# Kernel tuning notes

Measured on AMD Instinct MI355X. Metric: run time of the kernel, lower is better.

## Reference

```python
import jax, jax.numpy as jnp
import numpy as np

WS = 4          # window size per axis
HEADS = 3
HEAD_DIM = 32
DIM = 96
DISP = WS // 2  # displacement for shifted windows


def _make_mask(axis):
    # (w^3, w^3) additive mask, -inf across the wrap-around boundary on `axis`
    m = np.zeros((WS, WS, WS, WS, WS, WS), dtype=np.float32)
    d = DISP
    if axis == 0:
        m[-d:, :, :, :-d, :, :] = -np.inf
        m[:-d, :, :, -d:, :, :] = -np.inf
    elif axis == 1:
        m[:, -d:, :, :, :-d, :] = -np.inf
        m[:, :-d, :, :, -d:, :] = -np.inf
    else:
        m[:, :, -d:, :, :, :-d] = -np.inf
        m[:, :, :-d, :, :, -d:] = -np.inf
    return jnp.asarray(m.reshape(WS**3, WS**3))


def setup_inputs() -> dict:
    key = jax.random.key(0)
    k1, k2, k3, k4 = jax.random.split(key, 4)
    inner = HEADS * HEAD_DIM
    x = jax.random.normal(k1, (1, 64, 64, 64, DIM), dtype=jnp.float32)
    w_qkv = jax.random.normal(k2, (3 * inner, DIM), dtype=jnp.float32) * 0.02
    w_out = jax.random.normal(k3, (DIM, inner), dtype=jnp.float32) * 0.02
    b_out = jax.random.normal(k4, (DIM,), dtype=jnp.float32) * 0.02
    return {
        'x': x, 'w_qkv': w_qkv, 'w_out': w_out, 'b_out': b_out,
        'x_mask': _make_mask(0), 'y_mask': _make_mask(1), 'z_mask': _make_mask(2),
    }


def _forward(x, w_qkv, w_out, b_out, x_mask, y_mask, z_mask):
    scale = HEAD_DIM ** -0.5
    b, nx, ny, nz, _ = x.shape
    nwx, nwy, nwz = nx // WS, ny // WS, nz // WS
    seq = WS ** 3
    # cyclic shift by -displacement
    x = jnp.roll(x, shift=(-DISP, -DISP, -DISP), axis=(1, 2, 3))
    qkv = jnp.einsum('bxyzc,oc->bxyzo', x, w_qkv)
    q, k, v = jnp.split(qkv, 3, axis=-1)

    def win(t):  # -> (b, h, n_windows, seq, d)
        t = t.reshape(b, nwx, WS, nwy, WS, nwz, WS, HEADS, HEAD_DIM)
        t = t.transpose(0, 7, 1, 3, 5, 2, 4, 6, 8)
        return t.reshape(b, HEADS, nwx * nwy * nwz, seq, HEAD_DIM)

    q, k, v = win(q), win(k), win(v)
    dots = jnp.einsum('bhwid,bhwjd->bhwij', q, k) * scale

    # shifted-window masking (faithful to original einops relabeling, incl.
    # the final mislabeled rearrange which permutes the window grid)
    d = dots.reshape(b, HEADS, nwx, nwy, nwz, seq, seq)
    d = d.transpose(0, 1, 3, 4, 2, 5, 6)          # (b,h,ny,nz,nx,i,j)
    d = d.at[:, :, :, :, -1].add(x_mask)
    d = d.transpose(0, 1, 4, 3, 2, 5, 6)          # (b,h,nx,nz,ny,i,j)
    d = d.at[:, :, :, :, -1].add(y_mask)
    d = d.transpose(0, 1, 2, 4, 3, 5, 6)          # (b,h,nx,ny,nz,i,j)
    d = d.transpose(0, 1, 4, 2, 3, 5, 6)          # original's final rearrange bug
    dots = d.reshape(b, HEADS, nwx * nwy * nwz, seq, seq)

    attn = jax.nn.softmax(dots, axis=-1)
    out = jnp.einsum('bhwij,bhwjd->bhwid', attn, v)
    # un-window
    out = out.reshape(b, HEADS, nwx, nwy, nwz, WS, WS, WS, HEAD_DIM)
    out = out.transpose(0, 2, 5, 3, 6, 4, 7, 1, 8).reshape(b, nx, ny, nz, HEADS * HEAD_DIM)
    out = jnp.einsum('bxyzc,oc->bxyzo', out, w_out) + b_out
    # cyclic back shift
    return jnp.roll(out, shift=(DISP, DISP, DISP), axis=(1, 2, 3))


def reference(x, w_qkv, w_out, b_out, x_mask, y_mask, z_mask):
    return _forward(x, w_qkv, w_out, b_out, x_mask, y_mask, z_mask)
```

## Files before the change

### kernel.cpp

```cpp
#include <hip/hip_runtime.h>
#include <hip/hip_bf16.h>


using bf4   = __attribute__((ext_vector_type(4))) short;
using bf8   = __attribute__((ext_vector_type(8))) short;
using f32x4 = __attribute__((ext_vector_type(4))) float;

#define SW      100
#define WQ_ROWS 288
#define W_ROWS  384
#define W_SHORTS (W_ROWS * SW)

__device__ __forceinline__ short f2b(float f) {
  __hip_bfloat16 h = __float2bfloat16(f);
  return *reinterpret_cast<short*>(&h);
}
__device__ __forceinline__ bf4 pk4(const f32x4& a) {
  bf4 s; s[0] = f2b(a[0]); s[1] = f2b(a[1]); s[2] = f2b(a[2]); s[3] = f2b(a[3]);
  return s;
}
__device__ __forceinline__ bf4 pk4s(const f32x4& a, float sc) {
  bf4 s; s[0] = f2b(a[0] * sc); s[1] = f2b(a[1] * sc);
  s[2] = f2b(a[2] * sc); s[3] = f2b(a[3] * sc);
  return s;
}
__device__ __forceinline__ bf8 cvt8(const float4& a, const float4& b) {
  bf8 o;
  o[0] = f2b(a.x); o[1] = f2b(a.y); o[2] = f2b(a.z); o[3] = f2b(a.w);
  o[4] = f2b(b.x); o[5] = f2b(b.y); o[6] = f2b(b.z); o[7] = f2b(b.w);
  return o;
}

#if __has_builtin(__builtin_amdgcn_mfma_f32_16x16x16bf16_1k)
__device__ __forceinline__ f32x4 mfma16(bf4 a, bf4 b, f32x4 c) {
  return __builtin_amdgcn_mfma_f32_16x16x16bf16_1k(a, b, c, 0, 0, 0);
}
#elif __has_builtin(__builtin_amdgcn_mfma_f32_16x16x16_bf16)
__device__ __forceinline__ f32x4 mfma16(bf4 a, bf4 b, f32x4 c) {
  return __builtin_amdgcn_mfma_f32_16x16x16_bf16(a, b, c, 0, 0, 0);
}
#else
__device__ __forceinline__ f32x4 mfma16(bf4 a, bf4 b, f32x4 c) {
  asm("v_mfma_f32_16x16x16_bf16 %0, %1, %2, %0" : "+v"(c) : "v"(a), "v"(b));
  return c;
}
#endif

#if __has_builtin(__builtin_amdgcn_exp2f)
__device__ __forceinline__ float exp2n(float x) { return __builtin_amdgcn_exp2f(x); }
#else
__device__ __forceinline__ float exp2n(float x) {
  float r; asm("v_exp_f32 %0, %1" : "=v"(r) : "v"(x)); return r;
}
#endif

__global__ void prep_weights(const float* __restrict__ wq, const float* __restrict__ wo,
                             short* __restrict__ wpk) {
  int i = blockIdx.x * 256 + threadIdx.x;
  if (i >= W_SHORTS) return;
  int row = i / SW, c = i - row * SW;
  const float QS = 0.17677669529663687f * 1.4426950408889634f;
  float v = 0.f;
  if (c < 96) {
    if (row < 96)           v = wq[row * 96 + c] * QS;
    else if (row < WQ_ROWS) v = wq[row * 96 + c];
    else                    v = wo[(row - WQ_ROWS) * 96 + c];
  }
  wpk[i] = f2b(v);
}

__global__ __launch_bounds__(256)
__attribute__((amdgpu_waves_per_eu(1, 2)))
void fused_swin3d(const float* __restrict__ x,
                  const short* __restrict__ wpk,
                  const float* __restrict__ bo,
                  float* __restrict__ out) {
  __shared__ __align__(16) short ls_w[W_SHORTS];

  const int tid = threadIdx.x;
  const float4* wsrc = reinterpret_cast<const float4*>(wpk);
  #pragma unroll
  for (int i = 0; i < 19; ++i) {
    int c = i * 256 + tid;
    if (c < W_SHORTS / 8)
      *reinterpret_cast<float4*>(&ls_w[c * 8]) = wsrc[c];
  }

  const int wbase = ((int)blockIdx.x * 4 + (tid >> 6)) * 2;
  const int lane = tid & 63;
  const int lr   = lane & 15;
  const int kg   = lane >> 4;
  const int sy = (lr >> 2) & 3, sz = lr & 3;
  const int ch0 = kg * 8;
  const short* ls_wo = ls_w + WQ_ROWS * SW;

  __syncthreads();

  #pragma unroll
  for (int wi = 0; wi < 2; ++wi) {
    const int w = wbase + wi;
    const int p = w >> 8, q = (w >> 4) & 15, r = w & 15;

    bf4 qn[4][6], kn[4][6], vn[4][6];

    #pragma unroll
    for (int sc = 0; sc < 4; ++sc) {
      const int gx1 = (q * 4 + sc + 2) & 63, gy1 = (r * 4 + sy + 2) & 63, gz1 = (p * 4 + sz + 2) & 63;
      const size_t b1 = (size_t)((gx1 * 64 + gy1) * 64 + gz1) * 96;

      float4 xa0 = *reinterpret_cast<const float4*>(&x[b1 +  0 + ch0]);
      float4 xa1 = *reinterpret_cast<const float4*>(&x[b1 + 32 + ch0]);
      float4 xa2 = *reinterpret_cast<const float4*>(&x[b1 + 64 + ch0]);
      float4 xa3 = *reinterpret_cast<const float4*>(&x[b1 +  0 + ch0 + 4]);
      float4 xa4 = *reinterpret_cast<const float4*>(&x[b1 + 32 + ch0 + 4]);
      float4 xa5 = *reinterpret_cast<const float4*>(&x[b1 + 64 + ch0 + 4]);

      bf8 x1[3];
      x1[0] = cvt8(xa0, xa3); x1[1] = cvt8(xa1, xa4); x1[2] = cvt8(xa2, xa5);

      #pragma unroll
      for (int n = 0; n < 12; ++n) {
        f32x4 acc = {0.f, 0.f, 0.f, 0.f};
        const short* wrow = &ls_w[(n * 16 + lr) * SW + ch0];
        acc = __builtin_amdgcn_mfma_f32_16x16x32_bf16(*reinterpret_cast<const bf8*>(wrow +  0), x1[0], acc, 0, 0, 0);
        acc = __builtin_amdgcn_mfma_f32_16x16x32_bf16(*reinterpret_cast<const bf8*>(wrow + 32), x1[1], acc, 0, 0, 0);
        acc = __builtin_amdgcn_mfma_f32_16x16x32_bf16(*reinterpret_cast<const bf8*>(wrow + 64), x1[2], acc, 0, 0, 0);
        if (n < 6) qn[sc][n] = pk4(acc);
        else       kn[sc][n - 6] = pk4(acc);
      }
    }

    #pragma unroll
    for (int sc = 0; sc < 4; ++sc) {
      const int gx2 = (p * 4 + sc + 2) & 63, gy2 = (q * 4 + sy + 2) & 63, gz2 = (r * 4 + sz + 2) & 63;
      const size_t b2 = (size_t)((gx2 * 64 + gy2) * 64 + gz2) * 96;

      float4 xb0 = *reinterpret_cast<const float4*>(&x[b2 +  0 + ch0]);
      float4 xb1 = *reinterpret_cast<const float4*>(&x[b2 + 32 + ch0]);
      float4 xb2 = *reinterpret_cast<const float4*>(&x[b2 + 64 + ch0]);
      float4 xb3 = *reinterpret_cast<const float4*>(&x[b2 +  0 + ch0 + 4]);
      float4 xb4 = *reinterpret_cast<const float4*>(&x[b2 + 32 + ch0 + 4]);
      float4 xb5 = *reinterpret_cast<const float4*>(&x[b2 + 64 + ch0 + 4]);

      bf8 x2[3];
      x2[0] = cvt8(xb0, xb3); x2[1] = cvt8(xb1, xb4); x2[2] = cvt8(xb2, xb5);

      #pragma unroll
      for (int n = 0; n < 6; ++n) {
        f32x4 acc = {0.f, 0.f, 0.f, 0.f};
        const short* wrow = &ls_w[(192 + n * 16 + lr) * SW + ch0];
        acc = __builtin_amdgcn_mfma_f32_16x16x32_bf16(x2[0], *reinterpret_cast<const bf8*>(wrow +  0), acc, 0, 0, 0);
        acc = __builtin_amdgcn_mfma_f32_16x16x32_bf16(x2[1], *reinterpret_cast<const bf8*>(wrow + 32), acc, 0, 0, 0);
        acc = __builtin_amdgcn_mfma_f32_16x16x32_bf16(x2[2], *reinterpret_cast<const bf8*>(wrow + 64), acc, 0, 0, 0);
        vn[sc][n] = pk4(acc);
      }
    }

    const bool mx = (q == 15), my = (r == 15);
    const bool killy = my && ((lr >= 8) != (kg >= 2));

    #pragma unroll
    for (int qc = 0; qc < 4; ++qc) {
      f32x4 osw[6];
      #pragma unroll
      for (int c = 0; c < 6; ++c) osw[c] = (f32x4){0.f, 0.f, 0.f, 0.f};

      #pragma unroll
      for (int h = 0; h < 3; ++h) {
        f32x4 sv[4];
        __builtin_amdgcn_s_setprio(1);
        #pragma unroll
        for (int nj = 0; nj < 4; ++nj) {
          f32x4 z = {0.f, 0.f, 0.f, 0.f};
          z = mfma16(kn[nj][2 * h + 0], qn[qc][2 * h + 0], z);
          sv[nj] = mfma16(kn[nj][2 * h + 1], qn[qc][2 * h + 1], z);
        }
        __builtin_amdgcn_s_setprio(0);
        float ps[4];
        #pragma unroll
        for (int nj = 0; nj < 4; ++nj) {
          const bool kill = killy || (mx && ((qc >= 2) != (nj >= 2)));
          #pragma unroll
          for (int t = 0; t < 4; ++t)
            sv[nj][t] = kill ? 0.f : exp2n(sv[nj][t]);
          ps[nj] = (sv[nj][0] + sv[nj][1]) + (sv[nj][2] + sv[nj][3]);
        }
        float sum = (ps[0] + ps[1]) + (ps[2] + ps[3]);
        sum += __shfl_xor(sum, 16);
        sum += __shfl_xor(sum, 32);
        const float inv = 1.f / sum;
        bf4 pb[4];
        #pragma unroll
        for (int t = 0; t < 4; ++t) pb[t] = pk4s(sv[t], inv);
        __builtin_amdgcn_s_setprio(1);
        #pragma unroll
        for (int nc = 0; nc < 2; ++nc)
          #pragma unroll
          for (int t = 0; t < 4; ++t)
            osw[2 * h + nc] = mfma16(vn[t][2 * h + nc], pb[t], osw[2 * h + nc]);
        __builtin_amdgcn_s_setprio(0);
      }

      bf4 ofr[6];
      #pragma unroll
      for (int c = 0; c < 6; ++c) ofr[c] = pk4(osw[c]);

      const int gx2 = (p * 4 + qc + 2) & 63, gy2 = (q * 4 + sy + 2) & 63, gz2 = (r * 4 + sz + 2) & 63;
      const size_t b2 = (size_t)((gx2 * 64 + gy2) * 64 + gz2) * 96;
      #pragma unroll
      for (int no = 0; no < 6; ++no) {
        f32x4 acc = {0.f, 0.f, 0.f, 0.f};
        const short* wr = &ls_wo[(no * 16 + lr) * SW + kg * 4];
        #pragma unroll
        for (int c = 0; c < 6; ++c) {
          bf4 wa = *reinterpret_cast<const bf4*>(wr + c * 16);
          acc = mfma16(wa, ofr[c], acc);
        }
        const float4 bb = *reinterpret_cast<const float4*>(&bo[no * 16 + kg * 4]);
        float4 o4;
        o4.x = acc[0] + bb.x; o4.y = acc[1] + bb.y;
        o4.z = acc[2] + bb.z; o4.w = acc[3] + bb.w;
        *reinterpret_cast<float4*>(&out[b2 + no * 16 + kg * 4]) = o4;
      }
    }
  }
}

extern "C" void kernel_launch(void* const* d_in, const int* in_sizes, int n_in,
                              void* d_out, int out_size, void* d_ws, size_t ws_size,
                              hipStream_t stream) {
  const float* x  = (const float*)d_in[0];
  const float* wq = (const float*)d_in[1];
  const float* wo = (const float*)d_in[2];
  const float* bo = (const float*)d_in[3];

  short* wpk = (short*)d_ws;

  prep_weights<<<(W_SHORTS + 255) / 256, 256, 0, stream>>>(wq, wo, wpk);
  fused_swin3d<<<512, 256, 0, stream>>>(x, wpk, bo, (float*)d_out);
}
```

Measured before the change: 88.67 us.

## Use cheap bf16 packing and merge QK^T into single 16x16x32 MFMAs

Replaces per-element __float2bfloat16 conversions with a bit-add rounding trick that packs two floats per 32-bit word, cutting ALU work in every conversion. It also packs Q and K fragments as bf8 pairs, so each head's score computation uses one 16x16x32 MFMA instead of two chained 16x16x16 MFMAs. The rounding drops NaN handling and ties-to-even behaviour, which slightly changes numerics. The packing relies on the head-dim halves lining up with the K layout of the 32-wide MFMA.

Result: slower. 92.78 us (+4.6%).

```diff
diff --git a/kernel.cpp b/kernel.cpp
--- a/kernel.cpp
+++ b/kernel.cpp
@@ -11,25 +11,44 @@
 #define W_ROWS  384
 #define W_SHORTS (W_ROWS * SW)
 
+__device__ __forceinline__ unsigned rnd16(float f) {
+  return __builtin_bit_cast(unsigned, f) + 0x8000u;
+}
+__device__ __forceinline__ unsigned pk2u(float a, float b) {
+  return (rnd16(a) >> 16) | (rnd16(b) & 0xffff0000u);
+}
+__device__ __forceinline__ bf4 pk4f(const f32x4& v) {
+  union { unsigned u[2]; bf4 s; } t;
+  t.u[0] = pk2u(v[0], v[1]);
+  t.u[1] = pk2u(v[2], v[3]);
+  return t.s;
+}
+__device__ __forceinline__ bf4 pk4fs(const f32x4& v, float sc) {
+  f32x4 w = { v[0] * sc, v[1] * sc, v[2] * sc, v[3] * sc };
+  return pk4f(w);
+}
+__device__ __forceinline__ bf8 pk8f(const f32x4& a, const f32x4& b) {
+  union { unsigned u[4]; bf8 s; } t;
+  t.u[0] = pk2u(a[0], a[1]);
+  t.u[1] = pk2u(a[2], a[3]);
+  t.u[2] = pk2u(b[0], b[1]);
+  t.u[3] = pk2u(b[2], b[3]);
+  return t.s;
+}
+__device__ __forceinline__ bf8 cvt8f(const float4& a, const float4& b) {
+  union { unsigned u[4]; bf8 s; } t;
+  t.u[0] = pk2u(a.x, a.y);
+  t.u[1] = pk2u(a.z, a.w);
+  t.u[2] = pk2u(b.x, b.y);
+  t.u[3] = pk2u(b.z, b.w);
+  return t.s;
+}
 __device__ __forceinline__ short f2b(float f) {
   __hip_bfloat16 h = __float2bfloat16(f);
   return *reinterpret_cast<short*>(&h);
 }
-__device__ __forceinline__ bf4 pk4(const f32x4& a) {
-  bf4 s; s[0] = f2b(a[0]); s[1] = f2b(a[1]); s[2] = f2b(a[2]); s[3] = f2b(a[3]);
-  return s;
-}
-__device__ __forceinline__ bf4 pk4s(const f32x4& a, float sc) {
-  bf4 s; s[0] = f2b(a[0] * sc); s[1] = f2b(a[1] * sc);
-  s[2] = f2b(a[2] * sc); s[3] = f2b(a[3] * sc);
-  return s;
-}
-__device__ __forceinline__ bf8 cvt8(const float4& a, const float4& b) {
-  bf8 o;
-  o[0] = f2b(a.x); o[1] = f2b(a.y); o[2] = f2b(a.z); o[3] = f2b(a.w);
-  o[4] = f2b(b.x); o[5] = f2b(b.y); o[6] = f2b(b.z); o[7] = f2b(b.w);
-  return o;
-}
+
+#define mfma32 __builtin_amdgcn_mfma_f32_16x16x32_bf16
 
 #if __has_builtin(__builtin_amdgcn_mfma_f32_16x16x16bf16_1k)
 __device__ __forceinline__ f32x4 mfma16(bf4 a, bf4 b, f32x4 c) {
@@ -101,7 +120,8 @@
     const int w = wbase + wi;
     const int p = w >> 8, q = (w >> 4) & 15, r = w & 15;
 
-    bf4 qn[4][6], kn[4][6], vn[4][6];
+    bf8 qn8[4][3], kn8[4][3];
+    bf4 vn[4][6];
 
     #pragma unroll
     for (int sc = 0; sc < 4; ++sc) {
@@ -116,17 +136,23 @@
       float4 xa5 = *reinterpret_cast<const float4*>(&x[b1 + 64 + ch0 + 4]);
 
       bf8 x1[3];
-      x1[0] = cvt8(xa0, xa3); x1[1] = cvt8(xa1, xa4); x1[2] = cvt8(xa2, xa5);
-
-      #pragma unroll
-      for (int n = 0; n < 12; ++n) {
-        f32x4 acc = {0.f, 0.f, 0.f, 0.f};
-        const short* wrow = &ls_w[(n * 16 + lr) * SW + ch0];
-        acc = __builtin_amdgcn_mfma_f32_16x16x32_bf16(*reinterpret_cast<const bf8*>(wrow +  0), x1[0], acc, 0, 0, 0);
-        acc = __builtin_amdgcn_mfma_f32_16x16x32_bf16(*reinterpret_cast<const bf8*>(wrow + 32), x1[1], acc, 0, 0, 0);
-        acc = __builtin_amdgcn_mfma_f32_16x16x32_bf16(*reinterpret_cast<const bf8*>(wrow + 64), x1[2], acc, 0, 0, 0);
-        if (n < 6) qn[sc][n] = pk4(acc);
-        else       kn[sc][n - 6] = pk4(acc);
+      x1[0] = cvt8f(xa0, xa3); x1[1] = cvt8f(xa1, xa4); x1[2] = cvt8f(xa2, xa5);
+
+      #pragma unroll
+      for (int m = 0; m < 6; ++m) {
+        const int n0 = 2 * m, n1 = 2 * m + 1;
+        const short* w0 = &ls_w[(n0 * 16 + lr) * SW + ch0];
+        const short* w1 = &ls_w[(n1 * 16 + lr) * SW + ch0];
+        f32x4 a0 = {0.f, 0.f, 0.f, 0.f}, a1 = {0.f, 0.f, 0.f, 0.f};
+        a0 = mfma32(*reinterpret_cast<const bf8*>(w0 +  0), x1[0], a0, 0, 0, 0);
+        a0 = mfma32(*reinterpret_cast<const bf8*>(w0 + 32), x1[1], a0, 0, 0, 0);
+        a0 = mfma32(*reinterpret_cast<const bf8*>(w0 + 64), x1[2], a0, 0, 0, 0);
+        a1 = mfma32(*reinterpret_cast<const bf8*>(w1 +  0), x1[0], a1, 0, 0, 0);
+        a1 = mfma32(*reinterpret_cast<const bf8*>(w1 + 32), x1[1], a1, 0, 0, 0);
+        a1 = mfma32(*reinterpret_cast<const bf8*>(w1 + 64), x1[2], a1, 0, 0, 0);
+        bf8 pr = pk8f(a0, a1);
+        if (m < 3) qn8[sc][m] = pr;
+        else       kn8[sc][m - 3] = pr;
       }
     }
 
@@ -143,16 +169,16 @@
       float4 xb5 = *reinterpret_cast<const float4*>(&x[b2 + 64 + ch0 + 4]);
 
       bf8 x2[3];
-      x2[0] = cvt8(xb0, xb3); x2[1] = cvt8(xb1, xb4); x2[2] = cvt8(xb2, xb5);
+      x2[0] = cvt8f(xb0, xb3); x2[1] = cvt8f(xb1, xb4); x2[2] = cvt8f(xb2, xb5);
 
       #pragma unroll
       for (int n = 0; n < 6; ++n) {
         f32x4 acc = {0.f, 0.f, 0.f, 0.f};
         const short* wrow = &ls_w[(192 + n * 16 + lr) * SW + ch0];
-        acc = __builtin_amdgcn_mfma_f32_16x16x32_bf16(x2[0], *reinterpret_cast<const bf8*>(wrow +  0), acc, 0, 0, 0);
-        acc = __builtin_amdgcn_mfma_f32_16x16x32_bf16(x2[1], *reinterpret_cast<const bf8*>(wrow + 32), acc, 0, 0, 0);
-        acc = __builtin_amdgcn_mfma_f32_16x16x32_bf16(x2[2], *reinterpret_cast<const bf8*>(wrow + 64), acc, 0, 0, 0);
-        vn[sc][n] = pk4(acc);
+        acc = mfma32(x2[0], *reinterpret_cast<const bf8*>(wrow +  0), acc, 0, 0, 0);
+        acc = mfma32(x2[1], *reinterpret_cast<const bf8*>(wrow + 32), acc, 0, 0, 0);
+        acc = mfma32(x2[2], *reinterpret_cast<const bf8*>(wrow + 64), acc, 0, 0, 0);
+        vn[sc][n] = pk4f(acc);
       }
     }
 
@@ -172,8 +198,7 @@
         #pragma unroll
         for (int nj = 0; nj < 4; ++nj) {
           f32x4 z = {0.f, 0.f, 0.f, 0.f};
-          z = mfma16(kn[nj][2 * h + 0], qn[qc][2 * h + 0], z);
-          sv[nj] = mfma16(kn[nj][2 * h + 1], qn[qc][2 * h + 1], z);
+          sv[nj] = mfma32(kn8[nj][h], qn8[qc][h], z, 0, 0, 0);
         }
         __builtin_amdgcn_s_setprio(0);
         float ps[4];
@@ -191,7 +216,7 @@
         const float inv = 1.f / sum;
         bf4 pb[4];
         #pragma unroll
-        for (int t = 0; t < 4; ++t) pb[t] = pk4s(sv[t], inv);
+        for (int t = 0; t < 4; ++t) pb[t] = pk4fs(sv[t], inv);
         __builtin_amdgcn_s_setprio(1);
         #pragma unroll
         for (int nc = 0; nc < 2; ++nc)
@@ -203,7 +228,7 @@
 
       bf4 ofr[6];
       #pragma unroll
-      for (int c = 0; c < 6; ++c) ofr[c] = pk4(osw[c]);
+      for (int c = 0; c < 6; ++c) ofr[c] = pk4f(osw[c]);
 
       const int gx2 = (p * 4 + qc + 2) & 63, gy2 = (q * 4 + sy + 2) & 63, gz2 = (r * 4 + sz + 2) & 63;
       const size_t b2 = (size_t)((gx2 * 64 + gy2) * 64 + gz2) * 96;
```

## Prefetch window x loads before weight staging and across windows

Applied to the files above, without the earlier changes.

Window A's Q/K input loads are now issued before the weight copy into LDS, so global latency overlaps the LDS fill. Window B's Q/K input loads are issued and converted before window A's attention and output phase, hiding their latency behind compute. The loop body is split into helper functions for the QK projection, the V projection and the attention-plus-output stage. The cost is higher register pressure from holding prefetched data for two windows, which risks spills or lower occupancy.

Result: slower. 97.27 us (+9.7%).

```diff
diff --git a/kernel.cpp b/kernel.cpp
--- a/kernel.cpp
+++ b/kernel.cpp
@@ -30,6 +30,8 @@
   o[4] = f2b(b.x); o[5] = f2b(b.y); o[6] = f2b(b.z); o[7] = f2b(b.w);
   return o;
 }
+
+#define mfma32 __builtin_amdgcn_mfma_f32_16x16x32_bf16
 
 #if __has_builtin(__builtin_amdgcn_mfma_f32_16x16x16bf16_1k)
 __device__ __forceinline__ f32x4 mfma16(bf4 a, bf4 b, f32x4 c) {
@@ -69,6 +71,132 @@
   wpk[i] = f2b(v);
 }
 
+
+__device__ __forceinline__ void issue_xa_sc(const float* __restrict__ x,
+    int wx, int wy, int wz, int sc, int sy, int sz, int ch0, float4 fa[6]) {
+  const int gx = (wx * 4 + sc + 2) & 63, gy = (wy * 4 + sy + 2) & 63, gz = (wz * 4 + sz + 2) & 63;
+  const size_t b = (size_t)((gx * 64 + gy) * 64 + gz) * 96;
+  #pragma unroll
+  for (int f = 0; f < 3; ++f) {
+    fa[f]     = *reinterpret_cast<const float4*>(&x[b + f * 32 + ch0]);
+    fa[3 + f] = *reinterpret_cast<const float4*>(&x[b + f * 32 + ch0 + 4]);
+  }
+}
+__device__ __forceinline__ void cvt_sc(const float4 fa[6], bf8 x1[3]) {
+  x1[0] = cvt8(fa[0], fa[3]); x1[1] = cvt8(fa[1], fa[4]); x1[2] = cvt8(fa[2], fa[5]);
+}
+
+__device__ __forceinline__ void do_p1(const short* __restrict__ ls_w,
+    const bf8 x1[4][3], int lr, int ch0, bf4 qn[4][6], bf4 kn[4][6]) {
+  #pragma unroll
+  for (int sc = 0; sc < 4; ++sc) {
+    #pragma unroll
+    for (int n = 0; n < 12; ++n) {
+      f32x4 acc = {0.f, 0.f, 0.f, 0.f};
+      const short* wrow = &ls_w[(n * 16 + lr) * SW + ch0];
+      acc = mfma32(*reinterpret_cast<const bf8*>(wrow +  0), x1[sc][0], acc, 0, 0, 0);
+      acc = mfma32(*reinterpret_cast<const bf8*>(wrow + 32), x1[sc][1], acc, 0, 0, 0);
+      acc = mfma32(*reinterpret_cast<const bf8*>(wrow + 64), x1[sc][2], acc, 0, 0, 0);
+      if (n < 6) qn[sc][n] = pk4(acc);
+      else       kn[sc][n - 6] = pk4(acc);
+    }
+  }
+}
+
+__device__ __forceinline__ void do_p2(const float* __restrict__ x,
+    const short* __restrict__ ls_w, int p, int q, int r,
+    int sy, int sz, int ch0, int lr, bf4 vn[4][6]) {
+  #pragma unroll
+  for (int sc = 0; sc < 4; ++sc) {
+    float4 fb[6];
+    issue_xa_sc(x, p, q, r, sc, sy, sz, ch0, fb);
+    bf8 x2[3];
+    cvt_sc(fb, x2);
+    #pragma unroll
+    for (int n = 0; n < 6; ++n) {
+      f32x4 acc = {0.f, 0.f, 0.f, 0.f};
+      const short* wrow = &ls_w[(192 + n * 16 + lr) * SW + ch0];
+      acc = mfma32(x2[0], *reinterpret_cast<const bf8*>(wrow +  0), acc, 0, 0, 0);
+      acc = mfma32(x2[1], *reinterpret_cast<const bf8*>(wrow + 32), acc, 0, 0, 0);
+      acc = mfma32(x2[2], *reinterpret_cast<const bf8*>(wrow + 64), acc, 0, 0, 0);
+      vn[sc][n] = pk4(acc);
+    }
+  }
+}
+
+__device__ __forceinline__ void do_p34(const short* __restrict__ ls_wo,
+    const float* __restrict__ bo, float* __restrict__ out,
+    int p, int q, int r, int sy, int sz, int ch0, int lr, int kg,
+    const bf4 qn[4][6], const bf4 kn[4][6], const bf4 vn[4][6]) {
+  const bool mx = (q == 15), my = (r == 15);
+  const bool killy = my && ((lr >= 8) != (kg >= 2));
+
+  #pragma unroll
+  for (int qc = 0; qc < 4; ++qc) {
+    f32x4 osw[6];
+    #pragma unroll
+    for (int c = 0; c < 6; ++c) osw[c] = (f32x4){0.f, 0.f, 0.f, 0.f};
+
+    #pragma unroll
+    for (int h = 0; h < 3; ++h) {
+      f32x4 sv[4];
+      __builtin_amdgcn_s_setprio(1);
+      #pragma unroll
+      for (int nj = 0; nj < 4; ++nj) {
+        f32x4 z = {0.f, 0.f, 0.f, 0.f};
+        z = mfma16(kn[nj][2 * h + 0], qn[qc][2 * h + 0], z);
+        sv[nj] = mfma16(kn[nj][2 * h + 1], qn[qc][2 * h + 1], z);
+      }
+      __builtin_amdgcn_s_setprio(0);
+      float ps[4];
+      #pragma unroll
+      for (int nj = 0; nj < 4; ++nj) {
+        const bool kill = killy || (mx && ((qc >= 2) != (nj >= 2)));
+        #pragma unroll
+        for (int t = 0; t < 4; ++t)
+          sv[nj][t] = kill ? 0.f : exp2n(sv[nj][t]);
+        ps[nj] = (sv[nj][0] + sv[nj][1]) + (sv[nj][2] + sv[nj][3]);
+      }
+      float sum = (ps[0] + ps[1]) + (ps[2] + ps[3]);
+      sum += __shfl_xor(sum, 16);
+      sum += __shfl_xor(sum, 32);
+      const float inv = 1.f / sum;
+      bf4 pb[4];
+      #pragma unroll
+      for (int t = 0; t < 4; ++t) pb[t] = pk4s(sv[t], inv);
+      __builtin_amdgcn_s_setprio(1);
+      #pragma unroll
+      for (int nc = 0; nc < 2; ++nc)
+        #pragma unroll
+        for (int t = 0; t < 4; ++t)
+          osw[2 * h + nc] = mfma16(vn[t][2 * h + nc], pb[t], osw[2 * h + nc]);
+      __builtin_amdgcn_s_setprio(0);
+    }
+
+    bf4 ofr[6];
+    #pragma unroll
+    for (int c = 0; c < 6; ++c) ofr[c] = pk4(osw[c]);
+
+    const int gx2 = (p * 4 + qc + 2) & 63, gy2 = (q * 4 + sy + 2) & 63, gz2 = (r * 4 + sz + 2) & 63;
+    const size_t b2 = (size_t)((gx2 * 64 + gy2) * 64 + gz2) * 96;
+    #pragma unroll
+    for (int no = 0; no < 6; ++no) {
+      f32x4 acc = {0.f, 0.f, 0.f, 0.f};
+      const short* wr = &ls_wo[(no * 16 + lr) * SW + kg * 4];
+      #pragma unroll
+      for (int c = 0; c < 6; ++c) {
+        bf4 wa = *reinterpret_cast<const bf4*>(wr + c * 16);
+        acc = mfma16(wa, ofr[c], acc);
+      }
+      const float4 bb = *reinterpret_cast<const float4*>(&bo[no * 16 + kg * 4]);
+      float4 o4;
+      o4.x = acc[0] + bb.x; o4.y = acc[1] + bb.y;
+      o4.z = acc[2] + bb.z; o4.w = acc[3] + bb.w;
+      *reinterpret_cast<float4*>(&out[b2 + no * 16 + kg * 4]) = o4;
+    }
+  }
+}
+
 __global__ __launch_bounds__(256)
 __attribute__((amdgpu_waves_per_eu(1, 2)))
 void fused_swin3d(const float* __restrict__ x,
@@ -78,14 +206,6 @@
   __shared__ __align__(16) short ls_w[W_SHORTS];
 
   const int tid = threadIdx.x;
-  const float4* wsrc = reinterpret_cast<const float4*>(wpk);
-  #pragma unroll
-  for (int i = 0; i < 19; ++i) {
-    int c = i * 256 + tid;
-    if (c < W_SHORTS / 8)
-      *reinterpret_cast<float4*>(&ls_w[c * 8]) = wsrc[c];
-  }
-
   const int wbase = ((int)blockIdx.x * 4 + (tid >> 6)) * 2;
   const int lane = tid & 63;
   const int lr   = lane & 15;
@@ -94,136 +214,55 @@
   const int ch0 = kg * 8;
   const short* ls_wo = ls_w + WQ_ROWS * SW;
 
+  const int wA = wbase, wB = wbase + 1;
+  const int pA = wA >> 8, qA = (wA >> 4) & 15, rA = wA & 15;
+  const int pB = wB >> 8, qB = (wB >> 4) & 15, rB = wB & 15;
+
+  float4 faA[4][6];
+  #pragma unroll
+  for (int sc = 0; sc < 4; ++sc)
+    issue_xa_sc(x, qA, rA, pA, sc, sy, sz, ch0, faA[sc]);
+
+  const float4* wsrc = reinterpret_cast<const float4*>(wpk);
+  #pragma unroll
+  for (int i = 0; i < 19; ++i) {
+    int c = i * 256 + tid;
+    if (c < W_SHORTS / 8)
+      *reinterpret_cast<float4*>(&ls_w[c * 8]) = wsrc[c];
+  }
+
+  bf8 x1A[4][3];
+  #pragma unroll
+  for (int sc = 0; sc < 4; ++sc) cvt_sc(faA[sc], x1A[sc]);
+
   __syncthreads();
 
-  #pragma unroll
-  for (int wi = 0; wi < 2; ++wi) {
-    const int w = wbase + wi;
-    const int p = w >> 8, q = (w >> 4) & 15, r = w & 15;
-
-    bf4 qn[4][6], kn[4][6], vn[4][6];
-
-    #pragma unroll
-    for (int sc = 0; sc < 4; ++sc) {
-      const int gx1 = (q * 4 + sc + 2) & 63, gy1 = (r * 4 + sy + 2) & 63, gz1 = (p * 4 + sz + 2) & 63;
-      const size_t b1 = (size_t)((gx1 * 64 + gy1) * 64 + gz1) * 96;
-
-      float4 xa0 = *reinterpret_cast<const float4*>(&x[b1 +  0 + ch0]);
-      float4 xa1 = *reinterpret_cast<const float4*>(&x[b1 + 32 + ch0]);
-      float4 xa2 = *reinterpret_cast<const float4*>(&x[b1 + 64 + ch0]);
-      float4 xa3 = *reinterpret_cast<const float4*>(&x[b1 +  0 + ch0 + 4]);
-      float4 xa4 = *reinterpret_cast<const float4*>(&x[b1 + 32 + ch0 + 4]);
-      float4 xa5 = *reinterpret_cast<const float4*>(&x[b1 + 64 + ch0 + 4]);
-
-      bf8 x1[3];
-      x1[0] = cvt8(xa0, xa3); x1[1] = cvt8(xa1, xa4); x1[2] = cvt8(xa2, xa5);
-
-      #pragma unroll
-      for (int n = 0; n < 12; ++n) {
-        f32x4 acc = {0.f, 0.f, 0.f, 0.f};
-        const short* wrow = &ls_w[(n * 16 + lr) * SW + ch0];
-        acc = __builtin_amdgcn_mfma_f32_16x16x32_bf16(*reinterpret_cast<const bf8*>(wrow +  0), x1[0], acc, 0, 0, 0);
-        acc = __builtin_amdgcn_mfma_f32_16x16x32_bf16(*reinterpret_cast<const bf8*>(wrow + 32), x1[1], acc, 0, 0, 0);
-        acc = __builtin_amdgcn_mfma_f32_16x16x32_bf16(*reinterpret_cast<const bf8*>(wrow + 64), x1[2], acc, 0, 0, 0);
-        if (n < 6) qn[sc][n] = pk4(acc);
-        else       kn[sc][n - 6] = pk4(acc);
-      }
-    }
-
-    #pragma unroll
-    for (int sc = 0; sc < 4; ++sc) {
-      const int gx2 = (p * 4 + sc + 2) & 63, gy2 = (q * 4 + sy + 2) & 63, gz2 = (r * 4 + sz + 2) & 63;
-      const size_t b2 = (size_t)((gx2 * 64 + gy2) * 64 + gz2) * 96;
-
-      float4 xb0 = *reinterpret_cast<const float4*>(&x[b2 +  0 + ch0]);
-      float4 xb1 = *reinterpret_cast<const float4*>(&x[b2 + 32 + ch0]);
-      float4 xb2 = *reinterpret_cast<const float4*>(&x[b2 + 64 + ch0]);
-      float4 xb3 = *reinterpret_cast<const float4*>(&x[b2 +  0 + ch0 + 4]);
-      float4 xb4 = *reinterpret_cast<const float4*>(&x[b2 + 32 + ch0 + 4]);
-      float4 xb5 = *reinterpret_cast<const float4*>(&x[b2 + 64 + ch0 + 4]);
-
-      bf8 x2[3];
-      x2[0] = cvt8(xb0, xb3); x2[1] = cvt8(xb1, xb4); x2[2] = cvt8(xb2, xb5);
-
-      #pragma unroll
-      for (int n = 0; n < 6; ++n) {
-        f32x4 acc = {0.f, 0.f, 0.f, 0.f};
-        const short* wrow = &ls_w[(192 + n * 16 + lr) * SW + ch0];
-        acc = __builtin_amdgcn_mfma_f32_16x16x32_bf16(x2[0], *reinterpret_cast<const bf8*>(wrow +  0), acc, 0, 0, 0);
-        acc = __builtin_amdgcn_mfma_f32_16x16x32_bf16(x2[1], *reinterpret_cast<const bf8*>(wrow + 32), acc, 0, 0, 0);
-        acc = __builtin_amdgcn_mfma_f32_16x16x32_bf16(x2[2], *reinterpret_cast<const bf8*>(wrow + 64), acc, 0, 0, 0);
-        vn[sc][n] = pk4(acc);
-      }
-    }
-
-    const bool mx = (q == 15), my = (r == 15);
-    const bool killy = my && ((lr >= 8) != (kg >= 2));
-
-    #pragma unroll
-    for (int qc = 0; qc < 4; ++qc) {
-      f32x4 osw[6];
-      #pragma unroll
-      for (int c = 0; c < 6; ++c) osw[c] = (f32x4){0.f, 0.f, 0.f, 0.f};
-
-      #pragma unroll
-      for (int h = 0; h < 3; ++h) {
-        f32x4 sv[4];
-        __builtin_amdgcn_s_setprio(1);
-        #pragma unroll
-        for (int nj = 0; nj < 4; ++nj) {
-          f32x4 z = {0.f, 0.f, 0.f, 0.f};
-          z = mfma16(kn[nj][2 * h + 0], qn[qc][2 * h + 0], z);
-          sv[nj] = mfma16(kn[nj][2 * h + 1], qn[qc][2 * h + 1], z);
-        }
-        __builtin_amdgcn_s_setprio(0);
-        float ps[4];
-        #pragma unroll
-        for (int nj = 0; nj < 4; ++nj) {
-          const bool kill = killy || (mx && ((qc >= 2) != (nj >= 2)));
-          #pragma unroll
-          for (int t = 0; t < 4; ++t)
-            sv[nj][t] = kill ? 0.f : exp2n(sv[nj][t]);
-          ps[nj] = (sv[nj][0] + sv[nj][1]) + (sv[nj][2] + sv[nj][3]);
-        }
-        float sum = (ps[0] + ps[1]) + (ps[2] + ps[3]);
-        sum += __shfl_xor(sum, 16);
-        sum += __shfl_xor(sum, 32);
-        const float inv = 1.f / sum;
-        bf4 pb[4];
-        #pragma unroll
-        for (int t = 0; t < 4; ++t) pb[t] = pk4s(sv[t], inv);
-        __builtin_amdgcn_s_setprio(1);
-        #pragma unroll
-        for (int nc = 0; nc < 2; ++nc)
-          #pragma unroll
-          for (int t = 0; t < 4; ++t)
-            osw[2 * h + nc] = mfma16(vn[t][2 * h + nc], pb[t], osw[2 * h + nc]);
-        __builtin_amdgcn_s_setprio(0);
-      }
-
-      bf4 ofr[6];
-      #pragma unroll
-      for (int c = 0; c < 6; ++c) ofr[c] = pk4(osw[c]);
-
-      const int gx2 = (p * 4 + qc + 2) & 63, gy2 = (q * 4 + sy + 2) & 63, gz2 = (r * 4 + sz + 2) & 63;
-      const size_t b2 = (size_t)((gx2 * 64 + gy2) * 64 + gz2) * 96;
-      #pragma unroll
-      for (int no = 0; no < 6; ++no) {
-        f32x4 acc = {0.f, 0.f, 0.f, 0.f};
-        const short* wr = &ls_wo[(no * 16 + lr) * SW + kg * 4];
-        #pragma unroll
-        for (int c = 0; c < 6; ++c) {
-          bf4 wa = *reinterpret_cast<const bf4*>(wr + c * 16);
-          acc = mfma16(wa, ofr[c], acc);
-        }
-        const float4 bb = *reinterpret_cast<const float4*>(&bo[no * 16 + kg * 4]);
-        float4 o4;
-        o4.x = acc[0] + bb.x; o4.y = acc[1] + bb.y;
-        o4.z = acc[2] + bb.z; o4.w = acc[3] + bb.w;
-        *reinterpret_cast<float4*>(&out[b2 + no * 16 + kg * 4]) = o4;
-      }
-    }
-  }
+  bf4 qnA[4][6], knA[4][6], vnA[4][6];
+  do_p1(ls_w, x1A, lr, ch0, qnA, knA);
+  do_p2(x, ls_w, pA, qA, rA, sy, sz, ch0, lr, vnA);
+
+  bf8 x1B[4][3];
+  {
+    float4 f0[6], f1[6];
+    issue_xa_sc(x, qB, rB, pB, 0, sy, sz, ch0, f0);
+    issue_xa_sc(x, qB, rB, pB, 1, sy, sz, ch0, f1);
+    cvt_sc(f0, x1B[0]);
+    cvt_sc(f1, x1B[1]);
+  }
+  {
+    float4 f2[6], f3[6];
+    issue_xa_sc(x, qB, rB, pB, 2, sy, sz, ch0, f2);
+    issue_xa_sc(x, qB, rB, pB, 3, sy, sz, ch0, f3);
+    cvt_sc(f2, x1B[2]);
+    cvt_sc(f3, x1B[3]);
+  }
+
+  do_p34(ls_wo, bo, out, pA, qA, rA, sy, sz, ch0, lr, kg, qnA, knA, vnA);
+
+  bf4 qnB[4][6], knB[4][6], vnB[4][6];
+  do_p1(ls_w, x1B, lr, ch0, qnB, knB);
+  do_p2(x, ls_w, pB, qB, rB, sy, sz, ch0, lr, vnB);
+  do_p34(ls_wo, bo, out, pB, qB, rB, sy, sz, ch0, lr, kg, qnB, knB, vnB);
 }
 
 extern "C" void kernel_launch(void* const* d_in, const int* in_sizes, int n_in,
```
